# Kernel optimization log

Hardware: AMD Instinct MI355X
Metric: run time of the kernel (lower is better)

The kernel has to match this reference:

```python
import jax, jax.numpy as jnp
import numpy as np

B, T = 64, 256
IN, HID, OUT = 512, 1024, 256
NUM_DOMAINS = 20

def setup_inputs() -> dict:
    key = jax.random.key(0)
    k1, k2, k3, k4 = jax.random.split(key, 4)
    x = jax.random.normal(k1, (B, T, IN), dtype=jnp.float32)
    hetero_info = jax.random.randint(k2, (B, 2), 0, NUM_DOMAINS, dtype=jnp.int64)
    # embedding tables init N(0, 0.02) as in the torch module
    fc1_table = 0.02 * jax.random.normal(k3, (NUM_DOMAINS, IN * HID + HID), dtype=jnp.float32)
    fc2_table = 0.02 * jax.random.normal(k4, (NUM_DOMAINS, HID * OUT + OUT), dtype=jnp.float32)
    return {"x": x, "hetero_info": hetero_info, "fc1_table": fc1_table, "fc2_table": fc2_table}

def reference(x, hetero_info, fc1_table, fc2_table):
    domain_id = hetero_info[:, 0].astype(jnp.int32)
    Bn = domain_id.shape[0]
    fc1_param = fc1_table[domain_id]                     # (B, IN*HID + HID)
    w1 = fc1_param[:, : IN * HID].reshape(Bn, IN, HID)   # (B, IN, HID)
    b1 = fc1_param[:, IN * HID:].reshape(Bn, 1, HID)
    fc2_param = fc2_table[domain_id]                     # (B, HID*OUT + OUT)
    w2 = fc2_param[:, : HID * OUT].reshape(Bn, HID, OUT) # (B, HID, OUT)
    b2 = fc2_param[:, HID * OUT:].reshape(Bn, 1, OUT)
    h = jnp.einsum('bti,bih->bth', x, w1) + b1
    h = jax.nn.gelu(h, approximate=False)  # torch nn.GELU default = exact erf
    out = jnp.einsum('bth,bho->bto', h, w2) + b2
    return out
```

## Files before the change

kernel.cpp:

```cpp
#include <hip/hip_runtime.h>
#include <math.h>

#define B_  64
#define T_  256
#define IN_ 512
#define HID_ 1024
#define OUT_ 256
#define NDOM 20

typedef __bf16 bf16_t;
typedef __bf16 bf16x8 __attribute__((ext_vector_type(8)));
typedef float  f32x4  __attribute__((ext_vector_type(4)));

__device__ __forceinline__ unsigned f2bf_bits(float f) {
    unsigned u = __builtin_bit_cast(unsigned, f);
    return (u + 0x7FFFu + ((u >> 16) & 1u)) >> 16;
}
__device__ __forceinline__ unsigned pack_bf16x2(float x, float y) {
    return f2bf_bits(x) | (f2bf_bits(y) << 16);
}

__device__ __forceinline__ void gl_lds16(const void* g, void* l) {
    __builtin_amdgcn_global_load_lds(
        (const __attribute__((address_space(1))) unsigned*)g,
        (__attribute__((address_space(3))) unsigned*)l,
        16, 0, 0);
}

__global__ __launch_bounds__(256) void prepass(
    const float* __restrict__ X,  bf16_t* __restrict__ Xbf,
    const float* __restrict__ t1, bf16_t* __restrict__ W1t, float* __restrict__ b1,
    const float* __restrict__ t2, bf16_t* __restrict__ W2t, float* __restrict__ b2)
{
    const int bid = blockIdx.x;
    const int tid = threadIdx.x;

    if (bid < 8192) {
        const size_t idx = (size_t)bid * 256 + tid;
        float4 v = ((const float4*)X)[idx];
        uint2 p;
        p.x = pack_bf16x2(v.x, v.y);
        p.y = pack_bf16x2(v.z, v.w);
        ((uint2*)Xbf)[idx] = p;
        return;
    }

    __shared__ float t[64][65];

    const float* table; bf16_t* Wt; float* Bias;
    int K, N, d, n0, k0;
    if (bid < 10752) {
        const int r = bid - 8192;
        K = IN_; N = HID_;
        d = r >> 7;
        n0 = (r & 15) * 64;
        k0 = ((r >> 4) & 7) * 64;
        table = t1; Wt = W1t; Bias = b1;
    } else {
        const int r = bid - 10752;
        K = HID_; N = OUT_;
        d = r >> 6;
        n0 = (r & 3) * 64;
        k0 = ((r >> 2) & 15) * 64;
        table = t2; Wt = W2t; Bias = b2;
    }

    const float* W = table + (size_t)d * ((size_t)K * N + N);

    #pragma unroll
    for (int r = 0; r < 4; ++r) {
        const int kl = (tid >> 4) + r * 16;
        const int nl = (tid & 15) * 4;
        float4 v = *(const float4*)(W + (size_t)(k0 + kl) * N + n0 + nl);
        t[kl][nl + 0] = v.x; t[kl][nl + 1] = v.y;
        t[kl][nl + 2] = v.z; t[kl][nl + 3] = v.w;
    }
    __syncthreads();

    bf16_t* Wtd = Wt + (size_t)d * K * N;
    #pragma unroll
    for (int r = 0; r < 4; ++r) {
        const int nl = (tid >> 4) + r * 16;
        const int k4 = (tid & 15) * 4;
        uint2 p;
        p.x = pack_bf16x2(t[k4 + 0][nl], t[k4 + 1][nl]);
        p.y = pack_bf16x2(t[k4 + 2][nl], t[k4 + 3][nl]);
        *(uint2*)(Wtd + (size_t)(n0 + nl) * K + k0 + k4) = p;
    }

    if (k0 == 0 && tid < 64)
        Bias[(size_t)d * N + n0 + tid] = W[(size_t)K * N + n0 + tid];
}

#define CT_STRIDE 136
__global__ __launch_bounds__(256) void fc1_gemm(
    const bf16_t* __restrict__ Xbf,
    const bf16_t* __restrict__ W1t,
    const float*  __restrict__ Bias,
    const int*    __restrict__ hetero,
    bf16_t*       __restrict__ H)
{
    const int id   = blockIdx.x;
    const int g    = id & 255;
    const int nidx = id >> 8;
    const int b    = g >> 2;
    const int m0   = (g & 3) * 64;
    const int n0   = nidx * 128;
    const int d    = hetero[2 * b];
    const bf16_t* W    = W1t + (size_t)d * HID_ * IN_;
    const float*  bias = Bias + (size_t)d * HID_;
    const bf16_t* A    = Xbf + (size_t)(b * 256 + m0) * IN_;

    __shared__ __attribute__((aligned(16))) char smem[24576];
    bf16_t* LdsA = (bf16_t*)smem;
    bf16_t* LdsB = (bf16_t*)(smem + 8192);
    bf16_t* Ct   = (bf16_t*)smem;

    const int tid  = threadIdx.x;
    const int wave = tid >> 6;
    const int lane = tid & 63;
    const int l16  = lane & 15;
    const int quad = lane >> 4;
    const int wm   = (wave >> 1) * 32;
    const int wn   = (wave & 1) * 64;

    f32x4 acc[2][4] = {};

    for (int kk = 0; kk < IN_; kk += 64) {
        #pragma unroll
        for (int cc = 0; cc < 2; ++cc) {
            const int r0  = wave * 16 + cc * 8;
            const int row = r0 + (lane >> 3);
            const int cs  = (lane & 7) ^ (row & 7);
            gl_lds16(A + (size_t)row * IN_ + kk + cs * 8, &LdsA[r0 * 64]);
        }
        #pragma unroll
        for (int cc = 0; cc < 4; ++cc) {
            const int r0  = wave * 32 + cc * 8;
            const int row = r0 + (lane >> 3);
            const int cs  = (lane & 7) ^ (row & 7);
            gl_lds16(W + (size_t)(n0 + row) * IN_ + kk + cs * 8, &LdsB[r0 * 64]);
        }
        __syncthreads();

        #pragma unroll
        for (int h = 0; h < 2; ++h) {
            bf16x8 af[2], bfg[4];
            #pragma unroll
            for (int i = 0; i < 2; ++i) {
                const int r = wm + i * 16 + l16;
                const int c = (h * 4 + quad) ^ (r & 7);
                af[i] = *(const bf16x8*)&LdsA[r * 64 + c * 8];
            }
            #pragma unroll
            for (int j = 0; j < 4; ++j) {
                const int r = wn + j * 16 + l16;
                const int c = (h * 4 + quad) ^ (r & 7);
                bfg[j] = *(const bf16x8*)&LdsB[r * 64 + c * 8];
            }
            #pragma unroll
            for (int i = 0; i < 2; ++i)
                #pragma unroll
                for (int j = 0; j < 4; ++j)
                    acc[i][j] = __builtin_amdgcn_mfma_f32_16x16x32_bf16(bfg[j], af[i], acc[i][j], 0, 0, 0);
        }
        __syncthreads();
    }

    #pragma unroll
    for (int i = 0; i < 2; ++i) {
        const int m = wm + i * 16 + l16;
        #pragma unroll
        for (int j = 0; j < 4; ++j) {
            const int nl = wn + j * 16 + quad * 4;
            const float4 b4 = *(const float4*)&bias[n0 + nl];
            float v0 = acc[i][j][0] + b4.x;
            float v1 = acc[i][j][1] + b4.y;
            float v2 = acc[i][j][2] + b4.z;
            float v3 = acc[i][j][3] + b4.w;
            v0 = 0.5f * v0 * (1.0f + erff(v0 * 0.70710678f));
            v1 = 0.5f * v1 * (1.0f + erff(v1 * 0.70710678f));
            v2 = 0.5f * v2 * (1.0f + erff(v2 * 0.70710678f));
            v3 = 0.5f * v3 * (1.0f + erff(v3 * 0.70710678f));
            uint2 p;
            p.x = pack_bf16x2(v0, v1);
            p.y = pack_bf16x2(v2, v3);
            *(uint2*)&Ct[m * CT_STRIDE + nl] = p;
        }
    }
    __syncthreads();

    #pragma unroll
    for (int it = 0; it < 4; ++it) {
        const int row = it * 16 + (tid >> 4);
        const int ch  = tid & 15;
        uint4 v = *(const uint4*)&Ct[row * CT_STRIDE + ch * 8];
        *(uint4*)&H[((size_t)(b * 256 + m0 + row)) * HID_ + n0 + ch * 8] = v;
    }
}

__global__ __launch_bounds__(256) void fc2_gemm(
    const bf16_t* __restrict__ H,
    const bf16_t* __restrict__ W2t,
    const float*  __restrict__ Bias,
    const int*    __restrict__ hetero,
    float*        __restrict__ Out)
{
    const int id   = blockIdx.x;
    const int g    = id & 255;
    const int nidx = id >> 8;
    const int b    = g >> 2;
    const int m0   = (g & 3) * 64;
    const int n0   = nidx * 64;
    const int d    = hetero[2 * b];
    const bf16_t* W    = W2t + (size_t)d * OUT_ * HID_;
    const float*  bias = Bias + (size_t)d * OUT_;

    __shared__ __attribute__((aligned(16))) bf16_t LdsA[64 * 128];
    __shared__ __attribute__((aligned(16))) bf16_t LdsB[64 * 128];

    const int tid  = threadIdx.x;
    const int wave = tid >> 6;
    const int lane = tid & 63;
    const int l16  = lane & 15;
    const int quad = lane >> 4;
    const int wm   = (wave >> 1) * 32;
    const int wn   = (wave & 1) * 32;

    f32x4 acc[2][2] = {};

    for (int kk = 0; kk < HID_; kk += 128) {
        #pragma unroll
        for (int cc = 0; cc < 4; ++cc) {
            const int r0  = wave * 16 + cc * 4;
            const int row = r0 + (lane >> 4);
            const int cs  = (lane & 15) ^ (row & 15);
            gl_lds16(H + (size_t)(b * 256 + m0 + row) * HID_ + kk + cs * 8,
                     &LdsA[r0 * 128]);
        }
        #pragma unroll
        for (int cc = 0; cc < 4; ++cc) {
            const int r0  = wave * 16 + cc * 4;
            const int row = r0 + (lane >> 4);
            const int cs  = (lane & 15) ^ (row & 15);
            gl_lds16(W + (size_t)(n0 + row) * HID_ + kk + cs * 8,
                     &LdsB[r0 * 128]);
        }
        __syncthreads();

        #pragma unroll
        for (int h = 0; h < 4; ++h) {
            bf16x8 af[2], bfg[2];
            #pragma unroll
            for (int i = 0; i < 2; ++i) {
                const int r = wm + i * 16 + l16;
                const int c = (h * 4 + quad) ^ (r & 15);
                af[i] = *(const bf16x8*)&LdsA[r * 128 + c * 8];
            }
            #pragma unroll
            for (int j = 0; j < 2; ++j) {
                const int r = wn + j * 16 + l16;
                const int c = (h * 4 + quad) ^ (r & 15);
                bfg[j] = *(const bf16x8*)&LdsB[r * 128 + c * 8];
            }
            #pragma unroll
            for (int i = 0; i < 2; ++i)
                #pragma unroll
                for (int j = 0; j < 2; ++j)
                    acc[i][j] = __builtin_amdgcn_mfma_f32_16x16x32_bf16(bfg[j], af[i], acc[i][j], 0, 0, 0);
        }
        __syncthreads();
    }

    #pragma unroll
    for (int i = 0; i < 2; ++i) {
        const int m = m0 + wm + i * 16 + l16;
        #pragma unroll
        for (int j = 0; j < 2; ++j) {
            const int nl = wn + j * 16 + quad * 4;
            const float4 b4 = *(const float4*)&bias[n0 + nl];
            float4 o;
            o.x = acc[i][j][0] + b4.x;
            o.y = acc[i][j][1] + b4.y;
            o.z = acc[i][j][2] + b4.z;
            o.w = acc[i][j][3] + b4.w;
            *(float4*)&Out[(size_t)(b * 256 + m) * OUT_ + n0 + nl] = o;
        }
    }
}

extern "C" void kernel_launch(void* const* d_in, const int* in_sizes, int n_in,
                              void* d_out, int out_size, void* d_ws, size_t ws_size,
                              hipStream_t stream) {
    const float* x         = (const float*)d_in[0];
    const int*   hetero    = (const int*)d_in[1];
    const float* fc1_table = (const float*)d_in[2];
    const float* fc2_table = (const float*)d_in[3];
    float*       out       = (float*)d_out;

    char* ws = (char*)d_ws;
    bf16_t* W1t = (bf16_t*)(ws);
    bf16_t* W2t = (bf16_t*)(ws + 20971520);
    float*  b1  = (float*)(ws + 31457280);
    float*  b2  = (float*)(ws + 31539200);
    bf16_t* H   = (bf16_t*)(ws + 31559680);

    bf16_t* Xbf = (bf16_t*)d_out;

    prepass<<<dim3(12032), 256, 0, stream>>>(
        x, Xbf, fc1_table, W1t, b1, fc2_table, W2t, b2);

    fc1_gemm<<<dim3(2048), 256, 0, stream>>>(Xbf, W1t, b1, hetero, H);
    fc2_gemm<<<dim3(1024), 256, 0, stream>>>(H, W2t, b2, hetero, out);
}
```

Before: 192.9 us.

## Move fc2 weight conversion into fc1 GEMM launch to overlap with compute

The fc2 table transpose-and-convert-to-bf16 work moves out of the prepass kernel. It now runs as 1280 extra leading blocks of the fc1 GEMM launch. The memory-bound conversion can then overlap with the compute-bound fc1 GEMM instead of running serially before it. The trade-off is a divergent branch in the GEMM kernel and a shared LDS buffer reused as the transpose tile, which may affect register allocation or occupancy for the GEMM path.

```diff
diff --git a/kernel.cpp b/kernel.cpp
--- a/kernel.cpp
+++ b/kernel.cpp
@@ -27,10 +27,9 @@
         16, 0, 0);
 }
 
-__global__ __launch_bounds__(256) void prepass(
+__global__ __launch_bounds__(256) void prepassA(
     const float* __restrict__ X,  bf16_t* __restrict__ Xbf,
-    const float* __restrict__ t1, bf16_t* __restrict__ W1t, float* __restrict__ b1,
-    const float* __restrict__ t2, bf16_t* __restrict__ W2t, float* __restrict__ b2)
+    const float* __restrict__ t1, bf16_t* __restrict__ W1t, float* __restrict__ b1)
 {
     const int bid = blockIdx.x;
     const int tid = threadIdx.x;
@@ -47,60 +46,88 @@
 
     __shared__ float t[64][65];
 
-    const float* table; bf16_t* Wt; float* Bias;
-    int K, N, d, n0, k0;
-    if (bid < 10752) {
-        const int r = bid - 8192;
-        K = IN_; N = HID_;
-        d = r >> 7;
-        n0 = (r & 15) * 64;
-        k0 = ((r >> 4) & 7) * 64;
-        table = t1; Wt = W1t; Bias = b1;
-    } else {
-        const int r = bid - 10752;
-        K = HID_; N = OUT_;
-        d = r >> 6;
-        n0 = (r & 3) * 64;
-        k0 = ((r >> 2) & 15) * 64;
-        table = t2; Wt = W2t; Bias = b2;
-    }
-
-    const float* W = table + (size_t)d * ((size_t)K * N + N);
-
-    #pragma unroll
-    for (int r = 0; r < 4; ++r) {
-        const int kl = (tid >> 4) + r * 16;
+    const int r  = bid - 8192;
+    const int d  = r >> 7;
+    const int n0 = (r & 15) * 64;
+    const int k0 = ((r >> 4) & 7) * 64;
+    const float* W = t1 + (size_t)d * ((size_t)IN_ * HID_ + HID_);
+
+    #pragma unroll
+    for (int rr = 0; rr < 4; ++rr) {
+        const int kl = (tid >> 4) + rr * 16;
         const int nl = (tid & 15) * 4;
-        float4 v = *(const float4*)(W + (size_t)(k0 + kl) * N + n0 + nl);
+        float4 v = *(const float4*)(W + (size_t)(k0 + kl) * HID_ + n0 + nl);
         t[kl][nl + 0] = v.x; t[kl][nl + 1] = v.y;
         t[kl][nl + 2] = v.z; t[kl][nl + 3] = v.w;
     }
     __syncthreads();
 
-    bf16_t* Wtd = Wt + (size_t)d * K * N;
-    #pragma unroll
-    for (int r = 0; r < 4; ++r) {
-        const int nl = (tid >> 4) + r * 16;
+    bf16_t* Wtd = W1t + (size_t)d * IN_ * HID_;
+    #pragma unroll
+    for (int rr = 0; rr < 4; ++rr) {
+        const int nl = (tid >> 4) + rr * 16;
         const int k4 = (tid & 15) * 4;
         uint2 p;
         p.x = pack_bf16x2(t[k4 + 0][nl], t[k4 + 1][nl]);
         p.y = pack_bf16x2(t[k4 + 2][nl], t[k4 + 3][nl]);
-        *(uint2*)(Wtd + (size_t)(n0 + nl) * K + k0 + k4) = p;
+        *(uint2*)(Wtd + (size_t)(n0 + nl) * IN_ + k0 + k4) = p;
     }
 
     if (k0 == 0 && tid < 64)
-        Bias[(size_t)d * N + n0 + tid] = W[(size_t)K * N + n0 + tid];
+        b1[(size_t)d * HID_ + n0 + tid] = W[(size_t)IN_ * HID_ + n0 + tid];
 }
 
 #define CT_STRIDE 136
-__global__ __launch_bounds__(256) void fc1_gemm(
+__global__ __launch_bounds__(256) void fc1_w2cvt(
     const bf16_t* __restrict__ Xbf,
     const bf16_t* __restrict__ W1t,
     const float*  __restrict__ Bias,
     const int*    __restrict__ hetero,
-    bf16_t*       __restrict__ H)
+    bf16_t*       __restrict__ H,
+    const float*  __restrict__ t2,
+    bf16_t*       __restrict__ W2t,
+    float*        __restrict__ b2)
 {
-    const int id   = blockIdx.x;
+    const int bid = blockIdx.x;
+    const int tid = threadIdx.x;
+
+    __shared__ __attribute__((aligned(16))) char smem[24576];
+
+    if (bid < 1280) {
+        float (*t)[65] = (float(*)[65])smem;
+        const int r  = bid;
+        const int d  = r >> 6;
+        const int n0 = (r & 3) * 64;
+        const int k0 = ((r >> 2) & 15) * 64;
+        const float* W = t2 + (size_t)d * ((size_t)HID_ * OUT_ + OUT_);
+
+        #pragma unroll
+        for (int rr = 0; rr < 4; ++rr) {
+            const int kl = (tid >> 4) + rr * 16;
+            const int nl = (tid & 15) * 4;
+            float4 v = *(const float4*)(W + (size_t)(k0 + kl) * OUT_ + n0 + nl);
+            t[kl][nl + 0] = v.x; t[kl][nl + 1] = v.y;
+            t[kl][nl + 2] = v.z; t[kl][nl + 3] = v.w;
+        }
+        __syncthreads();
+
+        bf16_t* Wtd = W2t + (size_t)d * HID_ * OUT_;
+        #pragma unroll
+        for (int rr = 0; rr < 4; ++rr) {
+            const int nl = (tid >> 4) + rr * 16;
+            const int k4 = (tid & 15) * 4;
+            uint2 p;
+            p.x = pack_bf16x2(t[k4 + 0][nl], t[k4 + 1][nl]);
+            p.y = pack_bf16x2(t[k4 + 2][nl], t[k4 + 3][nl]);
+            *(uint2*)(Wtd + (size_t)(n0 + nl) * HID_ + k0 + k4) = p;
+        }
+
+        if (k0 == 0 && tid < 64)
+            b2[(size_t)d * OUT_ + n0 + tid] = W[(size_t)HID_ * OUT_ + n0 + tid];
+        return;
+    }
+
+    const int id   = bid - 1280;
     const int g    = id & 255;
     const int nidx = id >> 8;
     const int b    = g >> 2;
@@ -111,12 +138,10 @@
     const float*  bias = Bias + (size_t)d * HID_;
     const bf16_t* A    = Xbf + (size_t)(b * 256 + m0) * IN_;
 
-    __shared__ __attribute__((aligned(16))) char smem[24576];
     bf16_t* LdsA = (bf16_t*)smem;
     bf16_t* LdsB = (bf16_t*)(smem + 8192);
     bf16_t* Ct   = (bf16_t*)smem;
 
-    const int tid  = threadIdx.x;
     const int wave = tid >> 6;
     const int lane = tid & 63;
     const int l16  = lane & 15;
@@ -307,9 +332,10 @@
 
     bf16_t* Xbf = (bf16_t*)d_out;
 
-    prepass<<<dim3(12032), 256, 0, stream>>>(
-        x, Xbf, fc1_table, W1t, b1, fc2_table, W2t, b2);
-
-    fc1_gemm<<<dim3(2048), 256, 0, stream>>>(Xbf, W1t, b1, hetero, H);
+    prepassA<<<dim3(10752), 256, 0, stream>>>(x, Xbf, fc1_table, W1t, b1);
+
+    fc1_w2cvt<<<dim3(3328), 256, 0, stream>>>(
+        Xbf, W1t, b1, hetero, H, fc2_table, W2t, b2);
+
     fc2_gemm<<<dim3(1024), 256, 0, stream>>>(H, W2t, b2, hetero, out);
 }
```

Result: no change. 190.5 us (-1.3%).
